# Kernel tuning notes

Hardware: AMD Instinct MI355X
Metric: run time of the kernel (lower is better)

The kernel has to match this reference:

```python
import jax, jax.numpy as jnp
import numpy as np

N = 100000
E = 3200000
D_IN = 83
D_HID = 1024
N_CLASSES = 25


def setup_inputs() -> dict:
    key = jax.random.key(0)
    ks = jax.random.split(key, 10)
    feature = jax.random.normal(ks[0], (N, D_IN), dtype=jnp.float32)
    edge_row = jax.random.randint(ks[1], (E,), 0, N, dtype=jnp.int32)
    edge_col = jax.random.randint(ks[2], (E,), 0, N, dtype=jnp.int32)
    adj_val = jax.random.uniform(ks[3], (E,), dtype=jnp.float32)
    # Conv1d(1 -> 4, kernel 5, pad 2): weight [out=4, in=1, k=5]
    conv_w = jax.random.normal(ks[4], (4, 1, 5), dtype=jnp.float32) * 0.2
    conv_b = jnp.zeros((4,), dtype=jnp.float32)
    # GCN weights (kaiming-uniform-like scale), zero biases
    W1 = jax.random.uniform(ks[5], (D_IN, D_HID), dtype=jnp.float32,
                            minval=-1.0, maxval=1.0) * np.sqrt(6.0 / D_IN)
    b1 = jnp.zeros((D_HID,), dtype=jnp.float32)
    W2 = jax.random.uniform(ks[6], (D_HID, N_CLASSES), dtype=jnp.float32,
                            minval=-1.0, maxval=1.0) * np.sqrt(6.0 / D_HID)
    b2 = jnp.zeros((N_CLASSES,), dtype=jnp.float32)
    return {"feature": feature, "conv_w": conv_w, "conv_b": conv_b,
            "W1": W1, "b1": b1, "W2": W2, "b2": b2,
            "adj_val": adj_val, "edge_row": edge_row, "edge_col": edge_col}


def _spmm(vals, row, col, X):
    # sparse(adj) @ X : gather source rows, scale by edge value, scatter-add to dest
    return jax.ops.segment_sum(vals[:, None] * X[col], row, num_segments=N)


def reference(feature, conv_w, conv_b, W1, b1, W2, b2, adj_val, edge_row, edge_col):
    # Conv1d prelude: [N,1,83] -> [N,4,83], sum over channels, relu -> [N,83]
    x = jax.lax.conv_general_dilated(
        feature[:, None, :], conv_w, window_strides=(1,), padding=[(2, 2)],
        dimension_numbers=("NCH", "OIH", "NCH"))
    x = x + conv_b[None, :, None]
    x = jax.nn.relu(jnp.sum(x, axis=1))
    # GCN layer 1: relu(A @ (x W1) + b1)
    h = jax.nn.relu(_spmm(adj_val, edge_row, edge_col, x @ W1) + b1)
    # GCN layer 2: A @ (h W2) + b2
    logits = _spmm(adj_val, edge_row, edge_col, h @ W2) + b2
    return logits
```

## Files before the change

kernel.cpp:

```cpp
#include <hip/hip_runtime.h>

#define NN   100000
#define EE   3200000
#define DIN  83
#define DHID 1024
#define NCLS 25
#define XPAD 96
#define ZPAD 32

#define NBK     391
#define CHUNK   8192

typedef __attribute__((__ext_vector_type__(8))) short sh8;
typedef __attribute__((__ext_vector_type__(4))) float f4_t;

static __device__ __forceinline__ float relu_(float v) { return v > 0.f ? v : 0.f; }

static __device__ __forceinline__ unsigned short f2bf(float f) {
  unsigned int u = __float_as_uint(f);
  unsigned int r = u + 0x7FFFu + ((u >> 16) & 1u);
  return (unsigned short)(r >> 16);
}
static __device__ __forceinline__ float bflo(unsigned int q) {
  return __uint_as_float(q << 16);
}
static __device__ __forceinline__ float bfhi(unsigned int q) {
  return __uint_as_float(q & 0xFFFF0000u);
}

__global__ void conv_relu_k(const float* __restrict__ feature,
                            const float* __restrict__ conv_w,
                            const float* __restrict__ conv_b,
                            unsigned short* __restrict__ x) {
  float ws0 = conv_w[0] + conv_w[5] + conv_w[10] + conv_w[15];
  float ws1 = conv_w[1] + conv_w[6] + conv_w[11] + conv_w[16];
  float ws2 = conv_w[2] + conv_w[7] + conv_w[12] + conv_w[17];
  float ws3 = conv_w[3] + conv_w[8] + conv_w[13] + conv_w[18];
  float ws4 = conv_w[4] + conv_w[9] + conv_w[14] + conv_w[19];
  float bs  = conv_b[0] + conv_b[1] + conv_b[2] + conv_b[3];
  const int total = NN * XPAD;
  for (int idx = blockIdx.x * blockDim.x + threadIdx.x; idx < total;
       idx += gridDim.x * blockDim.x) {
    int n = idx / XPAD;
    int i = idx - n * XPAD;
    unsigned short o = 0;
    if (i < DIN) {
      const float* f = feature + (size_t)n * DIN;
      float acc = bs;
      if (i >= 2)      acc += ws0 * f[i - 2];
      if (i >= 1)      acc += ws1 * f[i - 1];
      acc += ws2 * f[i];
      if (i + 1 < DIN) acc += ws3 * f[i + 1];
      if (i + 2 < DIN) acc += ws4 * f[i + 2];
      o = f2bf(relu_(acc));
    }
    x[idx] = o;
  }
}

__global__ void prep_k(const float* __restrict__ W1, unsigned short* __restrict__ w1t,
                       const float* __restrict__ W2, unsigned short* __restrict__ w2t,
                       int* __restrict__ gbk) {
  int idx = blockIdx.x * blockDim.x + threadIdx.x;
  if (idx < DHID * XPAD) {
    int k = idx / DHID;
    int n = idx - k * DHID;
    float v = (k < DIN) ? W1[k * DHID + n] : 0.f;
    w1t[n * XPAD + k] = f2bf(v);
  }
  if (idx < 32 * DHID) {
    int k = idx / 32;
    int n = idx - k * 32;
    float v = (n < NCLS) ? W2[k * NCLS + n] : 0.f;
    w2t[n * DHID + k] = f2bf(v);
  }
  if (idx < NBK * 16) gbk[idx] = 0;
}


__global__ __launch_bounds__(256) void bucket_hist_k(
    const int* __restrict__ row, int* __restrict__ gbk) {
  __shared__ int cnt[NBK];
  const int tid = threadIdx.x;
  for (int b = tid; b < NBK; b += 256) cnt[b] = 0;
  __syncthreads();
  const int cb = blockIdx.x * CHUNK;
  const int csize = (cb + CHUNK <= EE) ? CHUNK : (EE - cb);
  for (int i = tid; i < csize; i += 256)
    atomicAdd(&cnt[row[cb + i] >> 8], 1);
  __syncthreads();
  for (int b = tid; b < NBK; b += 256)
    if (cnt[b]) atomicAdd(&gbk[b * 16], cnt[b]);
}

__global__ void scan_buckets_k(const int* __restrict__ gbk,
                               int* __restrict__ bbase, int* __restrict__ gcur) {
  __shared__ int sd[512];
  int t = threadIdx.x;
  int v = (t < NBK) ? gbk[t * 16] : 0;
  sd[t] = v;
  __syncthreads();
  for (int off = 1; off < 512; off <<= 1) {
    int add = (t >= off) ? sd[t - off] : 0;
    __syncthreads();
    sd[t] += add;
    __syncthreads();
  }
  if (t < NBK) {
    int excl = sd[t] - v;
    bbase[t] = excl;
    gcur[t * 16] = excl;
  }
  if (t == 0) bbase[NBK] = EE;
}

__global__ __launch_bounds__(256) void partition_k(
    const float* __restrict__ vals, const int* __restrict__ row,
    const int* __restrict__ col, int* __restrict__ gcur,
    int2* __restrict__ tmp) {
  __shared__ int cnt[NBK];
  __shared__ int sc[512];
  __shared__ int es[NBK + 1];
  __shared__ int lcur[NBK];
  __shared__ int gbase[NBK];
  __shared__ int2 staged[CHUNK];
  const int tid = threadIdx.x;
  const int cb = blockIdx.x * CHUNK;
  const int csize = (cb + CHUNK <= EE) ? CHUNK : (EE - cb);

  for (int b = tid; b < NBK; b += 256) cnt[b] = 0;
  __syncthreads();
  for (int i = tid; i < csize; i += 256)
    atomicAdd(&cnt[row[cb + i] >> 8], 1);
  __syncthreads();
  sc[tid]       = (tid < NBK) ? cnt[tid] : 0;
  sc[tid + 256] = (tid + 256 < NBK) ? cnt[tid + 256] : 0;
  __syncthreads();
  for (int off = 1; off < 512; off <<= 1) {
    int a0 = (tid >= off) ? sc[tid - off] : 0;
    int a1 = (tid + 256 >= off) ? sc[tid + 256 - off] : 0;
    __syncthreads();
    sc[tid] += a0;
    sc[tid + 256] += a1;
    __syncthreads();
  }
  for (int b = tid; b < NBK; b += 256) {
    int e = sc[b] - cnt[b];
    es[b] = e;
    lcur[b] = e;
  }
  if (tid == 0) es[NBK] = csize;
  __syncthreads();
  for (int b = tid; b < NBK; b += 256)
    gbase[b] = cnt[b] ? atomicAdd(&gcur[b * 16], cnt[b]) : 0;
  __syncthreads();
  for (int i = tid; i < csize; i += 256) {
    int r = row[cb + i];
    int lpos = atomicAdd(&lcur[r >> 8], 1);
    staged[lpos] = make_int2(col[cb + i] | ((r & 255) << 17),
                             __float_as_int(vals[cb + i]));
  }
  __syncthreads();
  {
    const int w = tid >> 6;
    const int lane = tid & 63;
    for (int b = w; b < NBK; b += 4) {
      int st = es[b], en = es[b + 1];
      int gb = gbase[b];
      for (int j = st + lane; j < en; j += 64)
        tmp[gb + (j - st)] = staged[j];
    }
  }
}

__global__ __launch_bounds__(256) void fine_scatter2_k(
    const int* __restrict__ bbase, const int2* __restrict__ tmp,
    int2* __restrict__ csr, int* __restrict__ offs, int* __restrict__ counts) {
  __shared__ int cnt[256];
  __shared__ int sd[256];
  __shared__ int lcur[256];
  const int tid = threadIdx.x;
  const int b = blockIdx.x;
  const int r0 = b * 256;
  const int gstart = bbase[b];
  const int nedge = bbase[b + 1] - gstart;
  cnt[tid] = 0;
  __syncthreads();
  for (int i = tid; i < nedge; i += 256)
    atomicAdd(&cnt[((unsigned)tmp[gstart + i].x) >> 17], 1);
  __syncthreads();
  int v = cnt[tid];
  sd[tid] = v;
  __syncthreads();
  for (int off = 1; off < 256; off <<= 1) {
    int add = (tid >= off) ? sd[tid - off] : 0;
    __syncthreads();
    sd[tid] += add;
    __syncthreads();
  }
  int excl = gstart + sd[tid] - v;
  int r = r0 + tid;
  if (r < NN) {
    offs[r] = excl;
    counts[r] = v;
  }
  lcur[tid] = excl;
  __syncthreads();
  for (int i = tid; i < nedge; i += 256) {
    int2 p = tmp[gstart + i];
    int rl = ((unsigned)p.x) >> 17;
    int pos = atomicAdd(&lcur[rl], 1);
    csr[pos] = make_int2(p.x & 0x1FFFF, p.y);
  }
}

__global__ __launch_bounds__(256) void spmm83_g(
    const int* __restrict__ offs, const int* __restrict__ cnt,
    const int2* __restrict__ csr, const unsigned short* __restrict__ x,
    unsigned short* __restrict__ ax) {
  int wave = (int)((blockIdx.x * blockDim.x + threadIdx.x) >> 6);
  int lane = threadIdx.x & 63;
  if (wave >= NN) return;
  int s = __builtin_amdgcn_readfirstlane(offs[wave]);
  int n = __builtin_amdgcn_readfirstlane(cnt[wave]);
  const bool act = lane < 48;
  const int d2 = lane * 2;
  float a0 = 0.f, a1 = 0.f;
  int i = 0;
  for (; i + 8 <= n; i += 8) {
    int2 p[8];
#pragma unroll
    for (int u = 0; u < 8; ++u) p[u] = csr[s + i + u];
    if (act) {
      unsigned int q[8];
#pragma unroll
      for (int u = 0; u < 8; ++u)
        q[u] = *(const unsigned int*)&x[(size_t)p[u].x * XPAD + d2];
#pragma unroll
      for (int u = 0; u < 8; ++u) {
        float v = __int_as_float(p[u].y);
        a0 += v * bflo(q[u]);
        a1 += v * bfhi(q[u]);
      }
    }
  }
  for (; i < n; ++i) {
    int2 p = csr[s + i];
    if (act) {
      unsigned int q = *(const unsigned int*)&x[(size_t)p.x * XPAD + d2];
      float v = __int_as_float(p.y);
      a0 += v * bflo(q);
      a1 += v * bfhi(q);
    }
  }
  if (act) {
    unsigned int o = (unsigned int)f2bf(a0) | ((unsigned int)f2bf(a1) << 16);
    *(unsigned int*)&ax[(size_t)wave * XPAD + d2] = o;
  }
}

__global__ __launch_bounds__(256) void spmm25_g(
    const int* __restrict__ offs, const int* __restrict__ cnt,
    const int2* __restrict__ csr, const unsigned short* __restrict__ zb,
    const float* __restrict__ b2, float* __restrict__ out) {
  int gw = (int)((blockIdx.x * blockDim.x + threadIdx.x) >> 6);
  int lane = threadIdx.x & 63;
  int sub = lane >> 4;
  int d2 = (lane & 15) * 2;
  int r = gw * 4 + sub;
  if (r >= NN) return;
  int s = offs[r];
  int n = cnt[r];
  float a0 = 0.f, a1 = 0.f;
  int i = 0;
  for (; i + 4 <= n; i += 4) {
    int2 p0 = csr[s + i + 0];
    int2 p1 = csr[s + i + 1];
    int2 p2 = csr[s + i + 2];
    int2 p3 = csr[s + i + 3];
    unsigned int q0 = *(const unsigned int*)&zb[(size_t)p0.x * ZPAD + d2];
    unsigned int q1 = *(const unsigned int*)&zb[(size_t)p1.x * ZPAD + d2];
    unsigned int q2 = *(const unsigned int*)&zb[(size_t)p2.x * ZPAD + d2];
    unsigned int q3 = *(const unsigned int*)&zb[(size_t)p3.x * ZPAD + d2];
    float v0 = __int_as_float(p0.y), v1 = __int_as_float(p1.y);
    float v2 = __int_as_float(p2.y), v3 = __int_as_float(p3.y);
    a0 += v0 * bflo(q0) + v1 * bflo(q1) + v2 * bflo(q2) + v3 * bflo(q3);
    a1 += v0 * bfhi(q0) + v1 * bfhi(q1) + v2 * bfhi(q2) + v3 * bfhi(q3);
  }
  for (; i < n; ++i) {
    int2 p = csr[s + i];
    unsigned int q = *(const unsigned int*)&zb[(size_t)p.x * ZPAD + d2];
    float v = __int_as_float(p.y);
    a0 += v * bflo(q);
    a1 += v * bfhi(q);
  }
  if (d2 < NCLS)     out[(size_t)r * NCLS + d2]     = a0 + b2[d2];
  if (d2 + 1 < NCLS) out[(size_t)r * NCLS + d2 + 1] = a1 + b2[d2 + 1];
}

__global__ __launch_bounds__(256) void fused_mlp_mfma(
    const unsigned short* __restrict__ axg, const unsigned short* __restrict__ w1t,
    const float* __restrict__ b1, const unsigned short* __restrict__ w2t,
    unsigned short* __restrict__ zb) {
  __shared__ __align__(16) unsigned short axs[128 * 104];
  __shared__ __align__(16) unsigned short hs[128 * 136];
  __shared__ float b1s[DHID];
  const int tid = threadIdx.x;
  const int n0 = blockIdx.x * 128;

  for (int idx = tid; idx < 128 * 12; idx += 256) {
    int m = idx / 12;
    int c8 = idx - m * 12;
    int node = n0 + m;
    sh8 v = {0, 0, 0, 0, 0, 0, 0, 0};
    if (node < NN) v = *(const sh8*)&axg[(size_t)node * XPAD + c8 * 8];
    *(sh8*)&axs[m * 104 + c8 * 8] = v;
  }
  for (int i = tid; i < DHID; i += 256) b1s[i] = b1[i];
  __syncthreads();

  const int lane = tid & 63;
  const int w = tid >> 6;
  const int quad = lane >> 4;
  const int tn = lane & 15;
  const int mta = w;
  const int mtb = w + 4;

  sh8 a1[8][3];
#pragma unroll
  for (int mt = 0; mt < 8; ++mt)
#pragma unroll
    for (int kc = 0; kc < 3; ++kc)
      a1[mt][kc] = *(const sh8*)&axs[(mt * 16 + tn) * 104 + kc * 32 + quad * 8];

  f4_t za0 = {0.f, 0.f, 0.f, 0.f}, za1 = {0.f, 0.f, 0.f, 0.f};
  f4_t zb0 = {0.f, 0.f, 0.f, 0.f}, zb1 = {0.f, 0.f, 0.f, 0.f};

  for (int c = 0; c < 8; ++c) {
    const int cb = c * 128;
#pragma unroll
    for (int nti = 0; nti < 2; ++nti) {
      const int nt = w * 2 + nti;
      const int ng = cb + nt * 16 + tn;
      const unsigned short* wr = &w1t[(size_t)ng * XPAD + quad * 8];
      sh8 b0 = *(const sh8*)&wr[0];
      sh8 b1f = *(const sh8*)&wr[32];
      sh8 b2f = *(const sh8*)&wr[64];
      float bias = b1s[ng];
#pragma unroll
      for (int mt = 0; mt < 8; ++mt) {
        f4_t acc = {0.f, 0.f, 0.f, 0.f};
        acc = __builtin_amdgcn_mfma_f32_16x16x32_bf16(a1[mt][0], b0, acc, 0, 0, 0);
        acc = __builtin_amdgcn_mfma_f32_16x16x32_bf16(a1[mt][1], b1f, acc, 0, 0, 0);
        acc = __builtin_amdgcn_mfma_f32_16x16x32_bf16(a1[mt][2], b2f, acc, 0, 0, 0);
#pragma unroll
        for (int r = 0; r < 4; ++r) {
          float v = relu_(acc[r] + bias);
          hs[(mt * 16 + quad * 4 + r) * 136 + nt * 16 + tn] = f2bf(v);
        }
      }
    }
    __syncthreads();
#pragma unroll
    for (int kc = 0; kc < 4; ++kc) {
      sh8 bl = *(const sh8*)&w2t[(size_t)tn * DHID + cb + kc * 32 + quad * 8];
      sh8 bh = *(const sh8*)&w2t[(size_t)(16 + tn) * DHID + cb + kc * 32 + quad * 8];
      sh8 aa = *(const sh8*)&hs[(mta * 16 + tn) * 136 + kc * 32 + quad * 8];
      za0 = __builtin_amdgcn_mfma_f32_16x16x32_bf16(aa, bl, za0, 0, 0, 0);
      za1 = __builtin_amdgcn_mfma_f32_16x16x32_bf16(aa, bh, za1, 0, 0, 0);
      sh8 ab = *(const sh8*)&hs[(mtb * 16 + tn) * 136 + kc * 32 + quad * 8];
      zb0 = __builtin_amdgcn_mfma_f32_16x16x32_bf16(ab, bl, zb0, 0, 0, 0);
      zb1 = __builtin_amdgcn_mfma_f32_16x16x32_bf16(ab, bh, zb1, 0, 0, 0);
    }
    __syncthreads();
  }

#pragma unroll
  for (int r = 0; r < 4; ++r) {
    int na = n0 + mta * 16 + quad * 4 + r;
    if (na < NN) {
      zb[(size_t)na * ZPAD + tn]      = f2bf(za0[r]);
      zb[(size_t)na * ZPAD + 16 + tn] = f2bf(za1[r]);
    }
    int nb = n0 + mtb * 16 + quad * 4 + r;
    if (nb < NN) {
      zb[(size_t)nb * ZPAD + tn]      = f2bf(zb0[r]);
      zb[(size_t)nb * ZPAD + 16 + tn] = f2bf(zb1[r]);
    }
  }
}

extern "C" void kernel_launch(void* const* d_in, const int* in_sizes, int n_in,
                              void* d_out, int out_size, void* d_ws, size_t ws_size,
                              hipStream_t stream) {
  const float* feature = (const float*)d_in[0];
  const float* conv_w  = (const float*)d_in[1];
  const float* conv_b  = (const float*)d_in[2];
  const float* W1      = (const float*)d_in[3];
  const float* b1      = (const float*)d_in[4];
  const float* W2      = (const float*)d_in[5];
  const float* b2      = (const float*)d_in[6];
  const float* adj     = (const float*)d_in[7];
  const int*   erow    = (const int*)d_in[8];
  const int*   ecol    = (const int*)d_in[9];
  float* out = (float*)d_out;

  char* B = (char*)d_ws;
  size_t o = 0;
  auto alloc = [&](size_t bytes, size_t align) -> void* {
    o = (o + align - 1) & ~(align - 1);
    void* p = B + o;
    o += bytes;
    return p;
  };
  unsigned short* x    = (unsigned short*)alloc((size_t)NN * XPAD * 2, 16);
  unsigned short* ax   = (unsigned short*)alloc((size_t)NN * XPAD * 2, 16);
  unsigned short* zb   = (unsigned short*)alloc((size_t)NN * ZPAD * 2, 16);
  int*   counts  = (int*)alloc((size_t)NN * 4, 16);
  int*   offs    = (int*)alloc((size_t)NN * 4, 16);
  int*   gcur    = (int*)alloc((size_t)NBK * 16 * 4, 64);
  int*   gbk     = (int*)alloc((size_t)NBK * 16 * 4, 64);
  int*   bbase   = (int*)alloc((size_t)(NBK + 1) * 4, 16);
  unsigned short* w1t = (unsigned short*)alloc((size_t)DHID * XPAD * 2, 16);
  unsigned short* w2t = (unsigned short*)alloc((size_t)32 * DHID * 2, 16);
  int2*  tmp     = (int2*)alloc((size_t)EE * 8, 16);
  int2*  csr     = (int2*)alloc((size_t)EE * 8, 16);

  conv_relu_k<<<8192, 256, 0, stream>>>(feature, conv_w, conv_b, x);
  prep_k<<<(DHID * XPAD + 255) / 256, 256, 0, stream>>>(W1, w1t, W2, w2t, gbk);
  bucket_hist_k<<<(EE + CHUNK - 1) / CHUNK, 256, 0, stream>>>(erow, gbk);
  scan_buckets_k<<<1, 512, 0, stream>>>(gbk, bbase, gcur);
  partition_k<<<(EE + CHUNK - 1) / CHUNK, 256, 0, stream>>>(adj, erow, ecol, gcur, tmp);
  fine_scatter2_k<<<NBK, 256, 0, stream>>>(bbase, tmp, csr, offs, counts);
  spmm83_g<<<(NN + 3) / 4, 256, 0, stream>>>(offs, counts, csr, x, ax);
  fused_mlp_mfma<<<(NN + 127) / 128, 256, 0, stream>>>(ax, w1t, b1, w2t, zb);
  spmm25_g<<<(NN + 15) / 16, 256, 0, stream>>>(offs, counts, csr, zb, b2, out);
}
```

Before: 479.0 us.

## Drop LDS staging in partition and widen histogram/scatter blocks to 512 threads

The partition kernel no longer stages edges in a 64KB shared buffer with a local prefix scan. It now writes each edge straight to its global bucket position, using a per-bucket cursor from the global atomic. This removes the scan, the extra barriers and the big LDS footprint, which should raise occupancy. The cost is scattered, uncoalesced global writes. Separately, the bucket histogram and fine scatter kernels move to 512-thread blocks for more parallelism per bucket.

New measurement: 472.1 us. No clear change (-1.4%).

```diff
diff --git a/kernel.cpp b/kernel.cpp
--- a/kernel.cpp
+++ b/kernel.cpp
@@ -78,18 +78,18 @@
 }
 
 
-__global__ __launch_bounds__(256) void bucket_hist_k(
+__global__ __launch_bounds__(512) void bucket_hist_k(
     const int* __restrict__ row, int* __restrict__ gbk) {
   __shared__ int cnt[NBK];
   const int tid = threadIdx.x;
-  for (int b = tid; b < NBK; b += 256) cnt[b] = 0;
+  for (int b = tid; b < NBK; b += 512) cnt[b] = 0;
   __syncthreads();
   const int cb = blockIdx.x * CHUNK;
   const int csize = (cb + CHUNK <= EE) ? CHUNK : (EE - cb);
-  for (int i = tid; i < csize; i += 256)
+  for (int i = tid; i < csize; i += 512)
     atomicAdd(&cnt[row[cb + i] >> 8], 1);
   __syncthreads();
-  for (int b = tid; b < NBK; b += 256)
+  for (int b = tid; b < NBK; b += 512)
     if (cnt[b]) atomicAdd(&gbk[b * 16], cnt[b]);
 }
 
@@ -119,11 +119,7 @@
     const int* __restrict__ col, int* __restrict__ gcur,
     int2* __restrict__ tmp) {
   __shared__ int cnt[NBK];
-  __shared__ int sc[512];
-  __shared__ int es[NBK + 1];
   __shared__ int lcur[NBK];
-  __shared__ int gbase[NBK];
-  __shared__ int2 staged[CHUNK];
   const int tid = threadIdx.x;
   const int cb = blockIdx.x * CHUNK;
   const int csize = (cb + CHUNK <= EE) ? CHUNK : (EE - cb);
@@ -133,47 +129,18 @@
   for (int i = tid; i < csize; i += 256)
     atomicAdd(&cnt[row[cb + i] >> 8], 1);
   __syncthreads();
-  sc[tid]       = (tid < NBK) ? cnt[tid] : 0;
-  sc[tid + 256] = (tid + 256 < NBK) ? cnt[tid + 256] : 0;
-  __syncthreads();
-  for (int off = 1; off < 512; off <<= 1) {
-    int a0 = (tid >= off) ? sc[tid - off] : 0;
-    int a1 = (tid + 256 >= off) ? sc[tid + 256 - off] : 0;
-    __syncthreads();
-    sc[tid] += a0;
-    sc[tid + 256] += a1;
-    __syncthreads();
-  }
-  for (int b = tid; b < NBK; b += 256) {
-    int e = sc[b] - cnt[b];
-    es[b] = e;
-    lcur[b] = e;
-  }
-  if (tid == 0) es[NBK] = csize;
-  __syncthreads();
   for (int b = tid; b < NBK; b += 256)
-    gbase[b] = cnt[b] ? atomicAdd(&gcur[b * 16], cnt[b]) : 0;
+    lcur[b] = cnt[b] ? atomicAdd(&gcur[b * 16], cnt[b]) : 0;
   __syncthreads();
   for (int i = tid; i < csize; i += 256) {
     int r = row[cb + i];
-    int lpos = atomicAdd(&lcur[r >> 8], 1);
-    staged[lpos] = make_int2(col[cb + i] | ((r & 255) << 17),
-                             __float_as_int(vals[cb + i]));
-  }
-  __syncthreads();
-  {
-    const int w = tid >> 6;
-    const int lane = tid & 63;
-    for (int b = w; b < NBK; b += 4) {
-      int st = es[b], en = es[b + 1];
-      int gb = gbase[b];
-      for (int j = st + lane; j < en; j += 64)
-        tmp[gb + (j - st)] = staged[j];
-    }
-  }
-}
-
-__global__ __launch_bounds__(256) void fine_scatter2_k(
+    int pos = atomicAdd(&lcur[r >> 8], 1);
+    tmp[pos] = make_int2(col[cb + i] | ((r & 255) << 17),
+                         __float_as_int(vals[cb + i]));
+  }
+}
+
+__global__ __launch_bounds__(512) void fine_scatter2_k(
     const int* __restrict__ bbase, const int2* __restrict__ tmp,
     int2* __restrict__ csr, int* __restrict__ offs, int* __restrict__ counts) {
   __shared__ int cnt[256];
@@ -184,29 +151,31 @@
   const int r0 = b * 256;
   const int gstart = bbase[b];
   const int nedge = bbase[b + 1] - gstart;
-  cnt[tid] = 0;
-  __syncthreads();
-  for (int i = tid; i < nedge; i += 256)
+  if (tid < 256) cnt[tid] = 0;
+  __syncthreads();
+  for (int i = tid; i < nedge; i += 512)
     atomicAdd(&cnt[((unsigned)tmp[gstart + i].x) >> 17], 1);
   __syncthreads();
-  int v = cnt[tid];
-  sd[tid] = v;
+  int v = 0;
+  if (tid < 256) { v = cnt[tid]; sd[tid] = v; }
   __syncthreads();
   for (int off = 1; off < 256; off <<= 1) {
-    int add = (tid >= off) ? sd[tid - off] : 0;
-    __syncthreads();
-    sd[tid] += add;
-    __syncthreads();
-  }
-  int excl = gstart + sd[tid] - v;
-  int r = r0 + tid;
-  if (r < NN) {
-    offs[r] = excl;
-    counts[r] = v;
-  }
-  lcur[tid] = excl;
-  __syncthreads();
-  for (int i = tid; i < nedge; i += 256) {
+    int add = (tid >= off && tid < 256) ? sd[tid - off] : 0;
+    __syncthreads();
+    if (tid < 256) sd[tid] += add;
+    __syncthreads();
+  }
+  if (tid < 256) {
+    int excl = gstart + sd[tid] - v;
+    int r = r0 + tid;
+    if (r < NN) {
+      offs[r] = excl;
+      counts[r] = v;
+    }
+    lcur[tid] = excl;
+  }
+  __syncthreads();
+  for (int i = tid; i < nedge; i += 512) {
     int2 p = tmp[gstart + i];
     int rl = ((unsigned)p.x) >> 17;
     int pos = atomicAdd(&lcur[rl], 1);
@@ -428,10 +397,10 @@
 
   conv_relu_k<<<8192, 256, 0, stream>>>(feature, conv_w, conv_b, x);
   prep_k<<<(DHID * XPAD + 255) / 256, 256, 0, stream>>>(W1, w1t, W2, w2t, gbk);
-  bucket_hist_k<<<(EE + CHUNK - 1) / CHUNK, 256, 0, stream>>>(erow, gbk);
+  bucket_hist_k<<<(EE + CHUNK - 1) / CHUNK, 512, 0, stream>>>(erow, gbk);
   scan_buckets_k<<<1, 512, 0, stream>>>(gbk, bbase, gcur);
   partition_k<<<(EE + CHUNK - 1) / CHUNK, 256, 0, stream>>>(adj, erow, ecol, gcur, tmp);
-  fine_scatter2_k<<<NBK, 256, 0, stream>>>(bbase, tmp, csr, offs, counts);
+  fine_scatter2_k<<<NBK, 512, 0, stream>>>(bbase, tmp, csr, offs, counts);
   spmm83_g<<<(NN + 3) / 4, 256, 0, stream>>>(offs, counts, csr, x, ax);
   fused_mlp_mfma<<<(NN + 127) / 128, 256, 0, stream>>>(ax, w1t, b1, w2t, zb);
   spmm25_g<<<(NN + 15) / 16, 256, 0, stream>>>(offs, counts, csr, zb, b2, out);
```
